# Kernel optimization log

Hardware: AMD Instinct MI355X
Metric: run time of the kernel (lower is better)

## Reference

```python
import jax, jax.numpy as jnp
import numpy as np

B, L, D = 16, 1024, 1024
H = 8
K = D // H
OUT = 64

def setup_inputs() -> dict:
    key = jax.random.key(0)
    ks = jax.random.split(key, 12)
    std = 0.1
    return {
        "x0": jax.random.normal(ks[0], (B, L, D), jnp.float32),
        "x1": jax.random.normal(ks[1], (B, L, D), jnp.float32),
        "x2": jax.random.normal(ks[2], (B, L, D), jnp.float32),
        "support": jax.random.normal(ks[3], (B, L), jnp.float32),
        "mask": jnp.ones((B, L), jnp.float32),
        "Wk": std * jax.random.normal(ks[4], (D, D), jnp.float32),   # tokeys.weight
        "Wq": std * jax.random.normal(ks[5], (D, D), jnp.float32),   # toqueries.weight
        "Wv": std * jax.random.normal(ks[6], (D, D), jnp.float32),   # tovalues.weight
        "Wu": std * jax.random.normal(ks[7], (D, D), jnp.float32),   # unifyheads.weight
        "bu": std * jax.random.normal(ks[8], (D,), jnp.float32),     # unifyheads.bias
        "Wmlp": std * jax.random.normal(ks[9], (OUT, D), jnp.float32),
        "bmlp": std * jax.random.normal(ks[10], (OUT,), jnp.float32),
    }

def reference(x0, x1, x2, support, mask, Wk, Wq, Wv, Wu, bu, Wmlp, bmlp):
    # SelfAttention with first=True: q from x2 via tokeys, k from x1 via toqueries, v from x0 via tovalues
    b, l, d = x0.shape
    h, k = H, K
    scale = k ** (-0.25)  # applied to both q and k, as in the torch code
    q = (x2 @ Wk.T).reshape(b, l, h, k) * scale
    key_ = (x1 @ Wq.T).reshape(b, l, h, k) * scale
    v = (x0 @ Wv.T).reshape(b, l, h, k)
    dot = jnp.einsum('blhk,bmhk->bhlm', q, key_)          # [b,h,l,l]
    attn = jax.nn.softmax(dot, axis=-1)
    out = jnp.einsum('bhlm,bmhk->blhk', attn, v).reshape(b, l, d)
    out = out @ Wu.T + bu                                  # unifyheads
    pooled = jnp.mean(out, axis=1) + jnp.max(out, axis=1)  # 'mean_and_max'
    logits = pooled @ Wmlp.T + bmlp                        # dropout = identity (eval)
    return logits
```

## Files before the change

kernel.cpp:

```cpp
#include <hip/hip_runtime.h>

using u16 = unsigned short;
using u32 = unsigned int;
using short8 = __attribute__((ext_vector_type(8))) short;
using floatx4 = __attribute__((ext_vector_type(4))) float;
using floatx16 = __attribute__((ext_vector_type(16))) float;
using u32x4 = __attribute__((ext_vector_type(4))) u32;

__device__ __forceinline__ u32 fbits(float f) { union { float f; u32 u; } v; v.f = f; return v.u; }
__device__ __forceinline__ float fofb(u32 u) { union { u32 u; float f; } v; v.u = u; return v.f; }

__device__ __forceinline__ u16 f2bf(float f) {
    u32 u = fbits(f);
    return (u16)((u + 0x7FFFu + ((u >> 16) & 1u)) >> 16);
}

__device__ __forceinline__ u32 cvtpk_bf16(float lo, float hi) {
    u32 r;
    asm("v_cvt_pk_bf16_f32 %0, %1, %2" : "=v"(r) : "v"(lo), "v"(hi));
    return r;
}

__device__ __forceinline__ void cvt_split8(const float* x, short8& h, short8& l) {
#pragma unroll
    for (int j = 0; j < 8; ++j) {
        u32 b = fbits(x[j]);
        h[j] = (short)(b >> 16);
        float r = x[j] - fofb(b & 0xffff0000u);
        l[j] = (short)(fbits(r) >> 16);
    }
}
__device__ __forceinline__ void cvt_rne8(const float* x, short8& h) {
#pragma unroll
    for (int j = 0; j < 8; ++j) h[j] = (short)f2bf(x[j]);
}

__device__ __forceinline__ void load_lds16(const void* g, u16* l) {
    __builtin_amdgcn_global_load_lds(
        (const __attribute__((address_space(1))) unsigned int*)(g),
        (__attribute__((address_space(3))) unsigned int*)(l), 16, 0, 0);
}

__device__ __forceinline__ void barrier_mem() {
    asm volatile("s_barrier" ::: "memory");
}
#define WAITVM(N) asm volatile("s_waitcnt vmcnt(" #N ")" ::: "memory")

template<bool DUP>
__global__ void convw_kernel(const float* __restrict__ W0, const float* __restrict__ W1,
                             const float* __restrict__ W2, const float* __restrict__ W3,
                             u16* __restrict__ D0, u16* __restrict__ D1,
                             u16* __restrict__ D2, u16* __restrict__ D3) {
    int y = blockIdx.y;
    const float* s = (y == 0) ? W0 : (y == 1) ? W1 : (y == 2) ? W2 : W3;
    u16* d = (y == 0) ? D0 : (y == 1) ? D1 : (y == 2) ? D2 : D3;
    int i = (blockIdx.x * 256 + threadIdx.x) * 4;
    float4 v = *reinterpret_cast<const float4*>(s + i);
    ushort4 h;
    h.x = f2bf(v.x); h.y = f2bf(v.y); h.z = f2bf(v.z); h.w = f2bf(v.w);
    if (DUP && y < 2) {
        int n = i >> 10, k = i & 1023;
        u16* base = d + (size_t)n * 2048 + k;
        *reinterpret_cast<ushort4*>(base) = h;
        *reinterpret_cast<ushort4*>(base + 1024) = h;
    } else {
        *reinterpret_cast<ushort4*>(d + i) = h;
    }
}

template<bool SPLIT>
__global__ __launch_bounds__(256)
void convx_kernel(const float* __restrict__ X, u16* __restrict__ O) {
    int i = (blockIdx.x * 256 + threadIdx.x) * 4;
    float4 v = *reinterpret_cast<const float4*>(X + i);
    if (SPLIT) {
        int m = i >> 10, k = i & 1023;
        float xs[4] = {v.x, v.y, v.z, v.w};
        ushort4 h, l;
        u16 hh[4], ll[4];
#pragma unroll
        for (int j = 0; j < 4; ++j) {
            u32 b = fbits(xs[j]);
            hh[j] = (u16)(b >> 16);
            float r = xs[j] - fofb(b & 0xffff0000u);
            ll[j] = (u16)(fbits(r) >> 16);
        }
        h.x = hh[0]; h.y = hh[1]; h.z = hh[2]; h.w = hh[3];
        l.x = ll[0]; l.y = ll[1]; l.z = ll[2]; l.w = ll[3];
        *reinterpret_cast<ushort4*>(O + (size_t)m * 2048 + k) = h;
        *reinterpret_cast<ushort4*>(O + (size_t)m * 2048 + 1024 + k) = l;
    } else {
        ushort4 h;
        h.x = f2bf(v.x); h.y = f2bf(v.y); h.z = f2bf(v.z); h.w = f2bf(v.w);
        *reinterpret_cast<ushort4*>(O + i) = h;
    }
}

template<int KDIM>
__device__ __forceinline__ void g256_stage(const u16* gA, const u16* gB, u16* sm,
                                           int buf, int t, int half, int wave8) {
    if (half < 2) {
#pragma unroll
        for (int i = 0; i < 2; ++i)
            load_lds16(gA + (size_t)(half * 128 + i * 64) * KDIM + t * 64,
                       sm + (buf * 2 + 0) * 16384 + (half * 128 + i * 64 + wave8) * 64);
    } else {
        int h = half - 2;
#pragma unroll
        for (int i = 0; i < 2; ++i)
            load_lds16(gB + (size_t)(h * 128 + i * 64) * KDIM + t * 64,
                       sm + (buf * 2 + 1) * 16384 + (h * 128 + i * 64 + wave8) * 64);
    }
}

template<int MH, int NH, bool READB, bool ENDBAR>
__device__ __forceinline__ void g256_phase(const u16* As, const u16* Bs,
                                           floatx4 (&acc)[8][4], short8 (&bfr)[2][2],
                                           int WR, int WC, int quad, int l15, int l7) {
    short8 afr[4][2];
#pragma unroll
    for (int mf = 0; mf < 4; ++mf)
#pragma unroll
        for (int ks = 0; ks < 2; ++ks)
            afr[mf][ks] = *reinterpret_cast<const short8*>(
                As + (WR * 128 + MH * 64 + mf * 16 + l15) * 64 + ((quad + 4 * ks) ^ l7) * 8);
    if (READB) {
#pragma unroll
        for (int nf = 0; nf < 2; ++nf)
#pragma unroll
            for (int ks = 0; ks < 2; ++ks)
                bfr[nf][ks] = *reinterpret_cast<const short8*>(
                    Bs + (WC * 64 + NH * 32 + nf * 16 + l15) * 64 + ((quad + 4 * ks) ^ l7) * 8);
    }
    barrier_mem();
    __builtin_amdgcn_s_setprio(1);
#pragma unroll
    for (int mf = 0; mf < 4; ++mf)
#pragma unroll
        for (int nf = 0; nf < 2; ++nf)
#pragma unroll
            for (int ks = 0; ks < 2; ++ks)
                acc[MH * 4 + mf][NH * 2 + nf] = __builtin_amdgcn_mfma_f32_16x16x32_bf16(
                    afr[mf][ks], bfr[nf][ks], acc[MH * 4 + mf][NH * 2 + nf], 0, 0, 0);
    __builtin_amdgcn_s_setprio(0);
    if (ENDBAR) barrier_mem();
}

template<int KDIM>
__global__ __launch_bounds__(512, 2)
void gemm256(const u16* __restrict__ A, const u16* __restrict__ B,
             u16* __restrict__ C, float scale)
{
    extern __shared__ u16 sm[];
    constexpr int NT = KDIM / 64;

    const int tid = threadIdx.x;
    const int lane = tid & 63, wave = tid >> 6;
    const int quad = lane >> 4, l15 = lane & 15, l7 = lane & 7;
    const int WR = wave >> 2, WC = wave & 3;
    const int wave8 = wave * 8;

    const int lin = blockIdx.x;
    const int xcd = lin & 7, j = lin >> 3;
    const int vbx = xcd * 8 + (j >> 2), vby = j & 3;
    const int bm = vbx * 256, bn = vby * 256;

    const int srow = wave8 + (lane >> 3);
    const int scg = (lane & 7) ^ ((lane >> 3) & 7);
    const u16* gA = A + (size_t)(bm + srow) * KDIM + scg * 8;
    const u16* gB = B + (size_t)(bn + srow) * KDIM + scg * 8;

    floatx4 acc[8][4];
#pragma unroll
    for (int mf = 0; mf < 8; ++mf)
#pragma unroll
        for (int nf = 0; nf < 4; ++nf)
#pragma unroll
            for (int r = 0; r < 4; ++r) acc[mf][nf][r] = 0.f;

#pragma unroll
    for (int h = 0; h < 4; ++h) g256_stage<KDIM>(gA, gB, sm, 0, 0, h, wave8);
    g256_stage<KDIM>(gA, gB, sm, 1, 1, 0, wave8);
    g256_stage<KDIM>(gA, gB, sm, 1, 1, 1, wave8);
    WAITVM(4);
    barrier_mem();

    short8 bfr[2][2];
#pragma unroll 1
    for (int t = 0; t < NT; ++t) {
        const int cur = t & 1, nxt = cur ^ 1;
        const u16* As = sm + cur * 32768;
        const u16* Bs = As + 16384;

        if (t + 1 < NT) g256_stage<KDIM>(gA, gB, sm, nxt, t + 1, 2, wave8);
        g256_phase<0, 0, true,  true>(As, Bs, acc, bfr, WR, WC, quad, l15, l7);
        if (t + 1 < NT) g256_stage<KDIM>(gA, gB, sm, nxt, t + 1, 3, wave8);
        g256_phase<1, 0, false, true>(As, Bs, acc, bfr, WR, WC, quad, l15, l7);
        g256_phase<0, 1, true,  true>(As, Bs, acc, bfr, WR, WC, quad, l15, l7);
        g256_phase<1, 1, false, false>(As, Bs, acc, bfr, WR, WC, quad, l15, l7);
        if (t + 2 < NT) {
            g256_stage<KDIM>(gA, gB, sm, cur, t + 2, 0, wave8);
            g256_stage<KDIM>(gA, gB, sm, cur, t + 2, 1, wave8);
        }
        if (t + 1 < NT) {
            if (t + 2 < NT) WAITVM(4);
            else            WAITVM(0);
        }
        barrier_mem();
    }

#pragma unroll
    for (int mf = 0; mf < 8; ++mf)
#pragma unroll
        for (int nf = 0; nf < 4; ++nf)
#pragma unroll
            for (int r = 0; r < 4; ++r) {
                int row = bm + WR * 128 + mf * 16 + quad * 4 + r;
                int col = bn + WC * 64 + nf * 16 + l15;
                C[(size_t)row * 1024 + col] = f2bf(acc[mf][nf][r] * scale);
            }
}

#define GN 1024

template<int KDIM, bool SPLIT, bool TRANS, bool POOL, bool FP32A>
__global__ __launch_bounds__(256)
void gemm_bt(const void* __restrict__ Av, const u16* __restrict__ Bh,
             u16* __restrict__ Cb, float scale, u16* __restrict__ Vt,
             float* __restrict__ psum, float* __restrict__ pmax)
{
    constexpr int SM = TRANS ? 17408 : (FP32A ? 12288 : 8192);
    __shared__ __align__(16) u16 smem[SM];

    const int tid  = threadIdx.x;
    const int lane = tid & 63, wave = tid >> 6;
    const int quad = lane >> 4, l15 = lane & 15;
    const int wr = wave >> 1, wc = wave & 1;
    const int bm = blockIdx.x * 128, bn = blockIdx.y * 128;

    const int BOff = FP32A ? 8192 : 4096;

    floatx4 acc[4][4];
#pragma unroll
    for (int mt = 0; mt < 4; ++mt)
#pragma unroll
        for (int nt = 0; nt < 4; ++nt)
#pragma unroll
            for (int r = 0; r < 4; ++r) acc[mt][nt][r] = 0.f;

    const int s8 = (quad ^ ((l15 >> 1) & 3)) * 8;

    for (int kt = 0; kt < KDIM; kt += 32) {
        __syncthreads();
        if (FP32A) {
            const float* Af = (const float*)Av;
            const int arow = lane >> 3, achk = (lane & 7) ^ (lane >> 3);
            const int brow = lane >> 2, bchk = (lane & 3) ^ ((lane >> 3) & 3);
#pragma unroll
            for (int j = 0; j < 6; ++j) {
                int n = wave + 4 * j;
                if (n < 16) {
                    load_lds16(Af + (size_t)(bm + n * 8 + arow) * KDIM + kt + achk * 4,
                               smem + n * 512);
                } else {
                    int m = n - 16;
                    load_lds16(Bh + (size_t)(bn + m * 16 + brow) * KDIM + kt + bchk * 8,
                               smem + 8192 + m * 512);
                }
            }
        } else {
            const u16* Ab = (const u16*)Av;
            const int cgl = (lane & 3) ^ ((lane >> 3) & 3);
            const int rl  = lane >> 2;
            const u16* gp = (wave < 2) ? Ab : Bh;
            int rowb = (wave < 2) ? bm : bn;
            u16* lp = smem + (wave >> 1) * 4096;
            int q0 = (wave & 1) * 4;
#pragma unroll
            for (int q = 0; q < 4; ++q) {
                int qq = q0 + q;
                load_lds16(gp + (size_t)(rowb + qq * 16 + rl) * KDIM + cgl * 8 + kt,
                           lp + qq * 512);
            }
        }
        __syncthreads();

        short8 a_h[4], a_l[4], b_h[4];
        if (FP32A) {
            const float* Af4 = (const float*)smem;
#pragma unroll
            for (int mt = 0; mt < 4; ++mt) {
                int ra = wr * 64 + mt * 16 + l15;
                int f = ra & 7;
                float xv[8];
                *reinterpret_cast<float4*>(xv) =
                    *reinterpret_cast<const float4*>(Af4 + ra * 32 + (((2 * quad) ^ f) * 4));
                *reinterpret_cast<float4*>(xv + 4) =
                    *reinterpret_cast<const float4*>(Af4 + ra * 32 + (((2 * quad + 1) ^ f) * 4));
                if (SPLIT) cvt_split8(xv, a_h[mt], a_l[mt]);
                else       cvt_rne8(xv, a_h[mt]);
            }
        } else {
#pragma unroll
            for (int mt = 0; mt < 4; ++mt) {
                int ra = wr * 64 + mt * 16 + l15;
                a_h[mt] = *reinterpret_cast<const short8*>(smem + ra * 32 + s8);
            }
        }
#pragma unroll
        for (int nt = 0; nt < 4; ++nt) {
            int rb = wc * 64 + nt * 16 + l15;
            b_h[nt] = *reinterpret_cast<const short8*>(smem + BOff + rb * 32 + s8);
        }
#pragma unroll
        for (int mt = 0; mt < 4; ++mt)
#pragma unroll
            for (int nt = 0; nt < 4; ++nt)
                acc[mt][nt] = __builtin_amdgcn_mfma_f32_16x16x32_bf16(a_h[mt], b_h[nt], acc[mt][nt], 0, 0, 0);
        if (SPLIT) {
#pragma unroll
            for (int mt = 0; mt < 4; ++mt)
#pragma unroll
                for (int nt = 0; nt < 4; ++nt)
                    acc[mt][nt] = __builtin_amdgcn_mfma_f32_16x16x32_bf16(a_l[mt], b_h[nt], acc[mt][nt], 0, 0, 0);
        }
    }

    if (POOL) {
#pragma unroll
        for (int nt = 0; nt < 4; ++nt) {
            float s = 0.f, m = -3.0e38f;
#pragma unroll
            for (int mt = 0; mt < 4; ++mt)
#pragma unroll
                for (int r = 0; r < 4; ++r) {
                    float v = acc[mt][nt][r];
                    s += v; m = fmaxf(m, v);
                }
            s += __shfl_xor(s, 16); s += __shfl_xor(s, 32);
            m = fmaxf(m, __shfl_xor(m, 16)); m = fmaxf(m, __shfl_xor(m, 32));
            if (quad == 0) {
                int col = bn + wc * 64 + nt * 16 + l15;
                int chunk = (bm >> 6) + wr;
                psum[chunk * 1024 + col] = s;
                pmax[chunk * 1024 + col] = m;
            }
        }
    } else if (!TRANS) {
#pragma unroll
        for (int mt = 0; mt < 4; ++mt)
#pragma unroll
            for (int nt = 0; nt < 4; ++nt)
#pragma unroll
                for (int r = 0; r < 4; ++r) {
                    int row = bm + wr * 64 + mt * 16 + quad * 4 + r;
                    int col = bn + wc * 64 + nt * 16 + l15;
                    Cb[(size_t)row * GN + col] = f2bf(acc[mt][nt][r] * scale);
                }
    } else {
        __syncthreads();
#pragma unroll
        for (int mt = 0; mt < 4; ++mt)
#pragma unroll
            for (int nt = 0; nt < 4; ++nt)
#pragma unroll
                for (int r = 0; r < 4; ++r) {
                    int row_local = wr * 64 + mt * 16 + quad * 4 + r;
                    int col_local = wc * 64 + nt * 16 + l15;
                    smem[col_local * 136 + row_local] = f2bf(acc[mt][nt][r]);
                }
        __syncthreads();
        int b = bm >> 10, l0 = bm & 1023, h = bn >> 7;
        int d = tid >> 1, rblk = (tid & 1) * 64;
        u16* gv = Vt + ((size_t)(b * 8 + h) * 128 + d) * 1024 + l0 + rblk;
#pragma unroll
        for (int v = 0; v < 8; ++v)
            *reinterpret_cast<short8*>(gv + v * 8) =
                *reinterpret_cast<const short8*>(smem + d * 136 + rblk + v * 8);
    }
}

#define LOG2E 1.44269504088896f
#define EXPC  46.1662413084470f

__global__ __launch_bounds__(256, 2)
void attn_kernel(const u16* __restrict__ Q, const u16* __restrict__ Kk,
                 const u16* __restrict__ Vt, u16* __restrict__ AO)
{
    __shared__ __align__(16) u16 Ks[2][64 * 128];
    __shared__ __align__(16) u16 Vts[2][128 * 64];

    const int tid  = threadIdx.x;
    const int lane = tid & 63, wave = tid >> 6;
    const int l31 = lane & 31, h2 = lane >> 5;
    const int l7 = lane & 7;

    const int lin = blockIdx.x + (blockIdx.y << 3) + (blockIdx.z << 6);
    const int qt = lin >> 7;
    const int hd = lin & 7;
    const int b  = (lin >> 3) & 15;

    short8 qf[8];
    {
        int qrow = b * 1024 + qt * 128 + wave * 32 + l31;
        const u16* qp = Q + (size_t)qrow * 1024 + hd * 128 + h2 * 8;
#pragma unroll
        for (int s = 0; s < 8; ++s)
            qf[s] = *reinterpret_cast<const short8*>(qp + s * 16);
    }

    float lsum = 0.f;
    floatx16 oacc[4];
#pragma unroll
    for (int db = 0; db < 4; ++db)
#pragma unroll
        for (int r = 0; r < 16; ++r) oacc[db][r] = 0.f;

    const int krow_l = lane >> 4;
    const u16* kgB[4];
#pragma unroll
    for (int i = 0; i < 4; ++i) {
        int cg = (lane & 15) ^ ((i * 4 + krow_l) & 7);
        kgB[i] = Kk + (size_t)(b * 1024 + wave * 16 + i * 4 + krow_l) * 1024
                    + hd * 128 + cg * 8;
    }
    const u16* vtb = Vt + (size_t)(b * 8 + hd) * 128 * 1024;
    const int vrow_l = lane >> 3;
    const u16* vgB = vtb + (size_t)(wave * 32 + vrow_l) * 1024
                         + (((lane & 7) ^ vrow_l) * 8);

#pragma unroll
    for (int i = 0; i < 4; ++i)
        load_lds16(kgB[i], &Ks[0][(wave * 16 + i * 4) * 128]);
#pragma unroll
    for (int i = 0; i < 4; ++i)
        load_lds16(vgB + (size_t)i * 8 * 1024, &Vts[0][(wave * 32 + i * 8) * 64]);

    for (int t = 0; t < 16; ++t) {
        const int cur = t & 1;
        asm volatile("s_waitcnt vmcnt(0)" ::: "memory");
        __builtin_amdgcn_s_barrier();
        __builtin_amdgcn_sched_barrier(0);
        if (t < 15) {
            const int nxt = cur ^ 1;
#pragma unroll
            for (int i = 0; i < 4; ++i)
                load_lds16(kgB[i] + (size_t)(t + 1) * 64 * 1024,
                           &Ks[nxt][(wave * 16 + i * 4) * 128]);
#pragma unroll
            for (int i = 0; i < 4; ++i)
                load_lds16(vgB + (size_t)i * 8 * 1024 + (size_t)(t + 1) * 64,
                           &Vts[nxt][(wave * 32 + i * 8) * 64]);
        }
        const u16* ksb = Ks[cur];
        const u16* vsb = Vts[cur];

        short8 pfr[4];
#pragma unroll
        for (int kb = 0; kb < 2; ++kb) {
            floatx16 sacc;
#pragma unroll
            for (int r = 0; r < 16; ++r) sacc[r] = 0.f;
            __builtin_amdgcn_s_setprio(1);
#pragma unroll
            for (int s = 0; s < 8; ++s) {
                short8 kfr = *reinterpret_cast<const short8*>(
                    &ksb[(kb * 32 + l31) * 128 + (((s * 2 + h2) ^ l7) * 8)]);
                sacc = __builtin_amdgcn_mfma_f32_32x32x16_bf16(kfr, qf[s], sacc, 0, 0, 0);
            }
            __builtin_amdgcn_s_setprio(0);
#pragma unroll
            for (int r = 0; r < 16; ++r) {
                float p = exp2f(fmaf(sacc[r], LOG2E, -EXPC));
                sacc[r] = p;
                lsum += p;
            }
            u32 c0[4], c1[4];
#pragma unroll
            for (int qd = 0; qd < 4; ++qd) {
                c0[qd] = cvtpk_bf16(sacc[4 * qd + 0], sacc[4 * qd + 1]);
                c1[qd] = cvtpk_bf16(sacc[4 * qd + 2], sacc[4 * qd + 3]);
            }
#pragma unroll
            for (int pb = 0; pb < 2; ++pb) {
                auto r1a = __builtin_amdgcn_permlane32_swap(c0[2 * pb],     c1[2 * pb],     false, false);
                auto r2a = __builtin_amdgcn_permlane32_swap(c1[2 * pb],     c0[2 * pb],     false, false);
                auto r1b = __builtin_amdgcn_permlane32_swap(c0[2 * pb + 1], c1[2 * pb + 1], false, false);
                auto r2b = __builtin_amdgcn_permlane32_swap(c1[2 * pb + 1], c0[2 * pb + 1], false, false);
                u32 w0 = h2 ? (u32)r2b[0] : (u32)r1a[0];
                u32 w1 = h2 ? (u32)r1b[0] : (u32)r2a[0];
                u32 w2 = h2 ? (u32)r2b[1] : (u32)r1a[1];
                u32 w3 = h2 ? (u32)r1b[1] : (u32)r2a[1];
                u32x4 ww = {w0, w1, w2, w3};
                pfr[kb * 2 + pb] = __builtin_bit_cast(short8, ww);
            }
        }

        __builtin_amdgcn_s_setprio(1);
#pragma unroll
        for (int ks = 0; ks < 4; ++ks) {
#pragma unroll
            for (int db = 0; db < 4; ++db) {
                int d = db * 32 + l31;
                short8 vfr = *reinterpret_cast<const short8*>(
                    &vsb[d * 64 + (((ks * 2 + h2) ^ l7) * 8)]);
                oacc[db] = __builtin_amdgcn_mfma_f32_32x32x16_bf16(pfr[ks], vfr, oacc[db], 0, 0, 0);
            }
        }
        __builtin_amdgcn_s_setprio(0);
    }

    lsum += __shfl_xor(lsum, 32);

    int qbase = b * 1024 + qt * 128 + wave * 32;
#pragma unroll
    for (int rg = 0; rg < 4; ++rg)
#pragma unroll
        for (int r = 0; r < 4; ++r) {
            int row = rg * 8 + 4 * h2 + r;
            float inv = 1.0f / __shfl(lsum, row);
            u16* ao = AO + (size_t)(qbase + row) * 1024 + hd * 128 + l31;
#pragma unroll
            for (int db = 0; db < 4; ++db)
                ao[db * 32] = f2bf(oacc[db][rg * 4 + r] * inv);
        }
}

__global__ __launch_bounds__(256)
void head_kernel(const float* __restrict__ psum, const float* __restrict__ pmax,
                 const float* __restrict__ bu, const float* __restrict__ Wmlp,
                 const float* __restrict__ bmlp, float* __restrict__ out) {
    __shared__ float pool_s[1024];
    int b = blockIdx.x, tid = threadIdx.x;
    int c4 = tid * 4;
    float4 s = {0.f, 0.f, 0.f, 0.f};
    float4 m = {-3.0e38f, -3.0e38f, -3.0e38f, -3.0e38f};
#pragma unroll
    for (int c = 0; c < 16; ++c) {
        float4 a = *reinterpret_cast<const float4*>(psum + (size_t)(b * 16 + c) * 1024 + c4);
        float4 x = *reinterpret_cast<const float4*>(pmax + (size_t)(b * 16 + c) * 1024 + c4);
        s.x += a.x; s.y += a.y; s.z += a.z; s.w += a.w;
        m.x = fmaxf(m.x, x.x); m.y = fmaxf(m.y, x.y);
        m.z = fmaxf(m.z, x.z); m.w = fmaxf(m.w, x.w);
    }
    float4 bb = *reinterpret_cast<const float4*>(bu + c4);
    pool_s[c4 + 0] = s.x * (1.0f / 1024.0f) + m.x + 2.0f * bb.x;
    pool_s[c4 + 1] = s.y * (1.0f / 1024.0f) + m.y + 2.0f * bb.y;
    pool_s[c4 + 2] = s.z * (1.0f / 1024.0f) + m.z + 2.0f * bb.z;
    pool_s[c4 + 3] = s.w * (1.0f / 1024.0f) + m.w + 2.0f * bb.w;
    __syncthreads();
    int o = tid >> 2, seg = tid & 3;
    const float4* wr = reinterpret_cast<const float4*>(Wmlp + o * 1024 + seg * 256);
    const float4* pr = reinterpret_cast<const float4*>(pool_s + seg * 256);
    float acc = 0.f;
#pragma unroll 8
    for (int i = 0; i < 64; ++i) {
        float4 a = pr[i], w = wr[i];
        acc += a.x * w.x + a.y * w.y + a.z * w.z + a.w * w.w;
    }
    acc += __shfl_xor(acc, 1);
    acc += __shfl_xor(acc, 2);
    if (seg == 0) out[b * 64 + o] = acc + bmlp[o];
}

extern "C" void kernel_launch(void* const* d_in, const int* in_sizes, int n_in,
                              void* d_out, int out_size, void* d_ws, size_t ws_size,
                              hipStream_t stream) {
    const float* x0 = (const float*)d_in[0];
    const float* x1 = (const float*)d_in[1];
    const float* x2 = (const float*)d_in[2];
    const float* Wk = (const float*)d_in[5];
    const float* Wq = (const float*)d_in[6];
    const float* Wv = (const float*)d_in[7];
    const float* Wu = (const float*)d_in[8];
    const float* bu = (const float*)d_in[9];
    const float* Wmlp = (const float*)d_in[10];
    const float* bmlp = (const float*)d_in[11];
    float* out = (float*)d_out;

    char* ws = (char*)d_ws;
    const size_t MB = 1048576ull;
    const float scale = 0.29730177875068026f;

    const size_t wo_new = 140 * MB;
    if (ws_size >= wo_new) {
        u16* Wk2 = (u16*)(ws);
        u16* Wq2 = (u16*)(ws + 4 * MB);
        u16* Wvh = (u16*)(ws + 8 * MB);
        u16* Wuh = (u16*)(ws + 10 * MB);
        u16* XS  = (u16*)(ws + 12 * MB);
        u16* Qb  = (u16*)(ws + 76 * MB);
        u16* Kb  = (u16*)(ws + 108 * MB);
        u16* Vt  = (u16*)(ws + 44 * MB);
        u16* AOb = XS;
        float* psum = (float*)Qb;
        float* pmax = (float*)((char*)Qb + 1 * MB);

        hipError_t attr_e = hipFuncSetAttribute(
            reinterpret_cast<const void*>(&gemm256<2048>),
            hipFuncAttributeMaxDynamicSharedMemorySize, 131072);
        const bool big = (attr_e == hipSuccess);

        convw_kernel<true><<<dim3(1024, 4), 256, 0, stream>>>(Wk, Wq, Wv, Wu, Wk2, Wq2, Wvh, Wuh);

        dim3 ggrid(128, 8);

        convx_kernel<true><<<16384, 256, 0, stream>>>(x2, XS);
        if (big) gemm256<2048><<<256, 512, 131072, stream>>>(XS, Wk2, Qb, scale);
        else     gemm_bt<2048, false, false, false, false><<<ggrid, 256, 0, stream>>>(XS, Wk2, Qb, scale, nullptr, nullptr, nullptr);

        convx_kernel<true><<<16384, 256, 0, stream>>>(x1, XS);
        if (big) gemm256<2048><<<256, 512, 131072, stream>>>(XS, Wq2, Kb, scale);
        else     gemm_bt<2048, false, false, false, false><<<ggrid, 256, 0, stream>>>(XS, Wq2, Kb, scale, nullptr, nullptr, nullptr);

        gemm_bt<1024, false, true, false, true><<<ggrid, 256, 0, stream>>>(x0, Wvh, nullptr, 1.0f, Vt, nullptr, nullptr);

        dim3 agrid(8, 8, 16);
        attn_kernel<<<agrid, 256, 0, stream>>>(Qb, Kb, Vt, AOb);

        gemm_bt<1024, false, false, true, false><<<ggrid, 256, 0, stream>>>(AOb, Wuh, nullptr, 1.0f, nullptr, psum, pmax);

        head_kernel<<<16, 256, 0, stream>>>(psum, pmax, bu, Wmlp, bmlp, out);
        return;
    }

    const size_t MB32 = 33554432ull;
    size_t wo = 0;
    u16* Wkh = (u16*)(ws + wo); wo += 2097152;
    u16* Wqh = (u16*)(ws + wo); wo += 2097152;
    u16* Wvh = (u16*)(ws + wo); wo += 2097152;
    u16* Wuh = (u16*)(ws + wo); wo += 2097152;
    u16* Qb = (u16*)(ws + wo); wo += MB32;
    u16* Kb = (u16*)(ws + wo); wo += MB32;
    u16* Vt = (u16*)(ws + wo); wo += MB32;
    u16* AOb = (u16*)(ws + wo); wo += MB32;
    float* psum = (float*)(ws + wo); wo += 1048576;
    float* pmax = (float*)(ws + wo); wo += 1048576;
    if (ws_size < wo) return;

    convw_kernel<false><<<dim3(1024, 4), 256, 0, stream>>>(Wk, Wq, Wv, Wu, Wkh, Wqh, Wvh, Wuh);

    dim3 ggrid(128, 8);
    gemm_bt<1024, true, false, false, true><<<ggrid, 256, 0, stream>>>(x2, Wkh, Qb, scale, nullptr, nullptr, nullptr);
    gemm_bt<1024, true, false, false, true><<<ggrid, 256, 0, stream>>>(x1, Wqh, Kb, scale, nullptr, nullptr, nullptr);
    gemm_bt<1024, false, true, false, true><<<ggrid, 256, 0, stream>>>(x0, Wvh, nullptr, 1.0f, Vt, nullptr, nullptr);

    dim3 agrid(8, 8, 16);
    attn_kernel<<<agrid, 256, 0, stream>>>(Qb, Kb, Vt, AOb);

    gemm_bt<1024, false, false, true, false><<<ggrid, 256, 0, stream>>>(AOb, Wuh, nullptr, 1.0f, nullptr, psum, pmax);

    head_kernel<<<16, 256, 0, stream>>>(psum, pmax, bu, Wmlp, bmlp, out);
}
```

Measured before the change: 592.9 us.

## Use 256x256 gemm kernel for V projection and unifyheads with fused epilogues

Extends the large 256x256-tile gemm kernel with two new epilogue modes: one writes V transposed per head through LDS, the other reduces columns to per-chunk sum and max for pooling. The V projection now goes through a bf16 conversion of x0 and this kernel, and the unifyheads projection also uses it. The head kernel takes a chunk count so it can consume the coarser pooling partials. This is meant to raise matmul efficiency on two GEMMs, at the cost of an extra conversion pass over x0 and an LDS round trip for the transposed V store.

```diff
diff --git a/kernel.cpp b/kernel.cpp
--- a/kernel.cpp
+++ b/kernel.cpp
@@ -146,10 +146,11 @@
     if (ENDBAR) barrier_mem();
 }
 
-template<int KDIM>
+template<int KDIM, int MODE>
 __global__ __launch_bounds__(512, 2)
 void gemm256(const u16* __restrict__ A, const u16* __restrict__ B,
-             u16* __restrict__ C, float scale)
+             u16* __restrict__ C, float scale, u16* __restrict__ Vt,
+             float* __restrict__ psum, float* __restrict__ pmax)
 {
     extern __shared__ u16 sm[];
     constexpr int NT = KDIM / 64;
@@ -209,16 +210,65 @@
         barrier_mem();
     }
 
-#pragma unroll
-    for (int mf = 0; mf < 8; ++mf)
-#pragma unroll
-        for (int nf = 0; nf < 4; ++nf)
-#pragma unroll
-            for (int r = 0; r < 4; ++r) {
-                int row = bm + WR * 128 + mf * 16 + quad * 4 + r;
+    if (MODE == 0) {
+#pragma unroll
+        for (int mf = 0; mf < 8; ++mf)
+#pragma unroll
+            for (int nf = 0; nf < 4; ++nf)
+#pragma unroll
+                for (int r = 0; r < 4; ++r) {
+                    int row = bm + WR * 128 + mf * 16 + quad * 4 + r;
+                    int col = bn + WC * 64 + nf * 16 + l15;
+                    C[(size_t)row * 1024 + col] = f2bf(acc[mf][nf][r] * scale);
+                }
+    } else if (MODE == 1) {
+        const int bb = bm >> 10, l0 = bm & 1023;
+        const int d = tid >> 2, seg = tid & 3;
+#pragma unroll
+        for (int pass = 0; pass < 2; ++pass) {
+            __syncthreads();
+            if ((WC >> 1) == pass) {
+#pragma unroll
+                for (int mf = 0; mf < 8; ++mf)
+#pragma unroll
+                    for (int nf = 0; nf < 4; ++nf)
+#pragma unroll
+                        for (int r = 0; r < 4; ++r) {
+                            int row_local = WR * 128 + mf * 16 + quad * 4 + r;
+                            int col_local = (WC & 1) * 64 + nf * 16 + l15;
+                            sm[col_local * 264 + row_local] = f2bf(acc[mf][nf][r]);
+                        }
+            }
+            __syncthreads();
+            int h = (bn >> 7) + pass;
+            u16* gv = Vt + ((size_t)(bb * 8 + h) * 128 + d) * 1024 + l0 + seg * 64;
+            const u16* ls = sm + d * 264 + seg * 64;
+#pragma unroll
+            for (int v = 0; v < 8; ++v)
+                *reinterpret_cast<short8*>(gv + v * 8) =
+                    *reinterpret_cast<const short8*>(ls + v * 8);
+        }
+    } else {
+#pragma unroll
+        for (int nf = 0; nf < 4; ++nf) {
+            float s = 0.f, m = -3.0e38f;
+#pragma unroll
+            for (int mf = 0; mf < 8; ++mf)
+#pragma unroll
+                for (int r = 0; r < 4; ++r) {
+                    float v = acc[mf][nf][r];
+                    s += v; m = fmaxf(m, v);
+                }
+            s += __shfl_xor(s, 16); s += __shfl_xor(s, 32);
+            m = fmaxf(m, __shfl_xor(m, 16)); m = fmaxf(m, __shfl_xor(m, 32));
+            if (quad == 0) {
                 int col = bn + WC * 64 + nf * 16 + l15;
-                C[(size_t)row * 1024 + col] = f2bf(acc[mf][nf][r] * scale);
-            }
+                int chunk = (bm >> 7) + WR;
+                psum[chunk * 1024 + col] = s;
+                pmax[chunk * 1024 + col] = m;
+            }
+        }
+    }
 }
 
 #define GN 1024
@@ -529,16 +579,15 @@
 __global__ __launch_bounds__(256)
 void head_kernel(const float* __restrict__ psum, const float* __restrict__ pmax,
                  const float* __restrict__ bu, const float* __restrict__ Wmlp,
-                 const float* __restrict__ bmlp, float* __restrict__ out) {
+                 const float* __restrict__ bmlp, float* __restrict__ out, int nch) {
     __shared__ float pool_s[1024];
     int b = blockIdx.x, tid = threadIdx.x;
     int c4 = tid * 4;
     float4 s = {0.f, 0.f, 0.f, 0.f};
     float4 m = {-3.0e38f, -3.0e38f, -3.0e38f, -3.0e38f};
-#pragma unroll
-    for (int c = 0; c < 16; ++c) {
-        float4 a = *reinterpret_cast<const float4*>(psum + (size_t)(b * 16 + c) * 1024 + c4);
-        float4 x = *reinterpret_cast<const float4*>(pmax + (size_t)(b * 16 + c) * 1024 + c4);
+    for (int c = 0; c < nch; ++c) {
+        float4 a = *reinterpret_cast<const float4*>(psum + (size_t)(b * nch + c) * 1024 + c4);
+        float4 x = *reinterpret_cast<const float4*>(pmax + (size_t)(b * nch + c) * 1024 + c4);
         s.x += a.x; s.y += a.y; s.z += a.z; s.w += a.w;
         m.x = fmaxf(m.x, x.x); m.y = fmaxf(m.y, x.y);
         m.z = fmaxf(m.z, x.z); m.w = fmaxf(m.w, x.w);
@@ -596,31 +645,46 @@
         float* psum = (float*)Qb;
         float* pmax = (float*)((char*)Qb + 1 * MB);
 
-        hipError_t attr_e = hipFuncSetAttribute(
-            reinterpret_cast<const void*>(&gemm256<2048>),
+        hipError_t e0 = hipFuncSetAttribute(
+            reinterpret_cast<const void*>(&gemm256<2048, 0>),
             hipFuncAttributeMaxDynamicSharedMemorySize, 131072);
-        const bool big = (attr_e == hipSuccess);
+        hipError_t e1 = hipFuncSetAttribute(
+            reinterpret_cast<const void*>(&gemm256<1024, 1>),
+            hipFuncAttributeMaxDynamicSharedMemorySize, 131072);
+        hipError_t e2 = hipFuncSetAttribute(
+            reinterpret_cast<const void*>(&gemm256<1024, 2>),
+            hipFuncAttributeMaxDynamicSharedMemorySize, 131072);
+        const bool big = (e0 == hipSuccess && e1 == hipSuccess && e2 == hipSuccess);
 
         convw_kernel<true><<<dim3(1024, 4), 256, 0, stream>>>(Wk, Wq, Wv, Wu, Wk2, Wq2, Wvh, Wuh);
 
-        dim3 ggrid(128, 8);
-
-        convx_kernel<true><<<16384, 256, 0, stream>>>(x2, XS);
-        if (big) gemm256<2048><<<256, 512, 131072, stream>>>(XS, Wk2, Qb, scale);
-        else     gemm_bt<2048, false, false, false, false><<<ggrid, 256, 0, stream>>>(XS, Wk2, Qb, scale, nullptr, nullptr, nullptr);
-
-        convx_kernel<true><<<16384, 256, 0, stream>>>(x1, XS);
-        if (big) gemm256<2048><<<256, 512, 131072, stream>>>(XS, Wq2, Kb, scale);
-        else     gemm_bt<2048, false, false, false, false><<<ggrid, 256, 0, stream>>>(XS, Wq2, Kb, scale, nullptr, nullptr, nullptr);
-
-        gemm_bt<1024, false, true, false, true><<<ggrid, 256, 0, stream>>>(x0, Wvh, nullptr, 1.0f, Vt, nullptr, nullptr);
-
-        dim3 agrid(8, 8, 16);
-        attn_kernel<<<agrid, 256, 0, stream>>>(Qb, Kb, Vt, AOb);
-
-        gemm_bt<1024, false, false, true, false><<<ggrid, 256, 0, stream>>>(AOb, Wuh, nullptr, 1.0f, nullptr, psum, pmax);
-
-        head_kernel<<<16, 256, 0, stream>>>(psum, pmax, bu, Wmlp, bmlp, out);
+        if (big) {
+            convx_kernel<true><<<16384, 256, 0, stream>>>(x2, XS);
+            gemm256<2048, 0><<<256, 512, 131072, stream>>>(XS, Wk2, Qb, scale, nullptr, nullptr, nullptr);
+            convx_kernel<true><<<16384, 256, 0, stream>>>(x1, XS);
+            gemm256<2048, 0><<<256, 512, 131072, stream>>>(XS, Wq2, Kb, scale, nullptr, nullptr, nullptr);
+
+            convx_kernel<false><<<16384, 256, 0, stream>>>(x0, XS);
+            gemm256<1024, 1><<<256, 512, 131072, stream>>>(XS, Wvh, nullptr, 1.0f, Vt, nullptr, nullptr);
+
+            dim3 agrid(8, 8, 16);
+            attn_kernel<<<agrid, 256, 0, stream>>>(Qb, Kb, Vt, AOb);
+
+            gemm256<1024, 2><<<256, 512, 131072, stream>>>(AOb, Wuh, nullptr, 1.0f, nullptr, psum, pmax);
+
+            head_kernel<<<16, 256, 0, stream>>>(psum, pmax, bu, Wmlp, bmlp, out, 8);
+        } else {
+            dim3 ggrid(128, 8);
+            convx_kernel<true><<<16384, 256, 0, stream>>>(x2, XS);
+            gemm_bt<2048, false, false, false, false><<<ggrid, 256, 0, stream>>>(XS, Wk2, Qb, scale, nullptr, nullptr, nullptr);
+            convx_kernel<true><<<16384, 256, 0, stream>>>(x1, XS);
+            gemm_bt<2048, false, false, false, false><<<ggrid, 256, 0, stream>>>(XS, Wq2, Kb, scale, nullptr, nullptr, nullptr);
+            gemm_bt<1024, false, true, false, true><<<ggrid, 256, 0, stream>>>(x0, Wvh, nullptr, 1.0f, Vt, nullptr, nullptr);
+            dim3 agrid(8, 8, 16);
+            attn_kernel<<<agrid, 256, 0, stream>>>(Qb, Kb, Vt, AOb);
+            gemm_bt<1024, false, false, true, false><<<ggrid, 256, 0, stream>>>(AOb, Wuh, nullptr, 1.0f, nullptr, psum, pmax);
+            head_kernel<<<16, 256, 0, stream>>>(psum, pmax, bu, Wmlp, bmlp, out, 16);
+        }
         return;
     }
 
@@ -650,5 +714,5 @@
 
     gemm_bt<1024, false, false, true, false><<<ggrid, 256, 0, stream>>>(AOb, Wuh, nullptr, 1.0f, nullptr, psum, pmax);
 
-    head_kernel<<<16, 256, 0, stream>>>(psum, pmax, bu, Wmlp, bmlp, out);
-}
+    head_kernel<<<16, 256, 0, stream>>>(psum, pmax, bu, Wmlp, bmlp, out, 16);
+}
```

Result: faster. 546.7 us (-7.8%).
